# Kernel optimization log

Measured on AMD Instinct MI355X. Metric: run time of the kernel, lower is better.

Reference implementation:

```python
import jax, jax.numpy as jnp
import numpy as np


def setup_inputs() -> dict:
    key = jax.random.key(0)
    kq, kk, kv = jax.random.split(key, 3)
    n, d = 8192, 128
    Q = jax.random.normal(kq, (n, d), dtype=jnp.float32)
    K = jax.random.normal(kk, (n, d), dtype=jnp.float32)
    V = jax.random.normal(kv, (n, d), dtype=jnp.float32)
    return {"Q": Q, "K": K, "V": V}


def reference(Q, K, V):
    # The blockwise online-softmax loops in the torch module compute exactly
    # softmax(Q @ K^T) @ V  -- note: NO 1/sqrt(d) scaling in the original.
    S = jnp.einsum('qd,kd->qk', Q, K)          # [n, n] scores
    P = jax.nn.softmax(S, axis=-1)             # numerically stable softmax
    O = jnp.einsum('qk,kd->qd', P, V)          # [n, d]
    return O
```

## Files before the change

### kernel.cpp

```cpp
#include <hip/hip_runtime.h>
#include <hip/hip_bf16.h>

#define N 8192
#define D 128
#define NSPLIT 8
#define KVSPLIT (N / NSPLIT)
#define KVBLK 64
#define NT (KVSPLIT / KVBLK)

typedef __attribute__((ext_vector_type(8))) _Float16 half8;
typedef __attribute__((ext_vector_type(2))) __fp16 fp16x2;
typedef __attribute__((ext_vector_type(16))) float f32x16;

union H8 { fp16x2 h2[4]; half8 h8; };

__global__ void cvt_f16_4(const float4* __restrict__ src, _Float16* __restrict__ dst, int n4) {
    int i = blockIdx.x * 256 + threadIdx.x;
    if (i < n4) {
        float4 v = src[i];
        _Float16 o0 = (_Float16)v.x, o1 = (_Float16)v.y, o2 = (_Float16)v.z, o3 = (_Float16)v.w;
        ushort4 o;
        o.x = __builtin_bit_cast(ushort, o0);
        o.y = __builtin_bit_cast(ushort, o1);
        o.z = __builtin_bit_cast(ushort, o2);
        o.w = __builtin_bit_cast(ushort, o3);
        *reinterpret_cast<ushort4*>(dst + i * 4) = o;
    }
}

__global__ void transpose_v(const float* __restrict__ V, _Float16* __restrict__ Vtp) {
    __shared__ _Float16 tile[64][65];
    const int k0 = blockIdx.x * 64;
    const int d0 = blockIdx.y * 64;
    const int tid = threadIdx.x;
#pragma unroll
    for (int p = 0; p < 16; ++p) {
        int flat = p * 256 + tid;
        int r = flat >> 6, cc = flat & 63;
        tile[r][cc] = (_Float16)(V[(size_t)(k0 + r) * D + d0 + cc]);
    }
    __syncthreads();
#pragma unroll
    for (int p = 0; p < 16; ++p) {
        int flat = p * 256 + tid;
        int dd = flat >> 6, kl = flat & 63;
        int kk = kl & 31;
        int s32 = 16 * (kk >> 4) + 8 * ((kk >> 2) & 1) + 4 * ((kk >> 3) & 1) + (kk & 3);
        Vtp[(size_t)(d0 + dd) * N + k0 + (kl & 32) + s32] = tile[kl][dd];
    }
}

#define STAGE(kdst_, vdst_, kbase_)                                                   \
    {                                                                                 \
        _Pragma("unroll")                                                             \
        for (int p = 0; p < 4; ++p) {                                                 \
            int c4 = p * 256 + tid;                                                   \
            int row = c4 >> 4, chs = c4 & 15;                                         \
            int cc = (chs & 8) | ((chs & 7) ^ (row & 7));                             \
            __builtin_amdgcn_global_load_lds(                                         \
                (const __attribute__((address_space(1))) void*)(Kh + (size_t)((kbase_) + row) * D + cc * 8), \
                (__attribute__((address_space(3))) void*)((kdst_) + c4 * 8), 16, 0, 0);              \
        }                                                                             \
        _Pragma("unroll")                                                             \
        for (int p = 0; p < 4; ++p) {                                                 \
            int c4 = p * 256 + tid;                                                   \
            int dd = c4 >> 3, chs = c4 & 7;                                           \
            int cc = chs ^ (dd & 7);                                                  \
            __builtin_amdgcn_global_load_lds(                                         \
                (const __attribute__((address_space(1))) void*)(Vtp + (size_t)dd * N + (kbase_) + cc * 8),   \
                (__attribute__((address_space(3))) void*)((vdst_) + c4 * 8), 16, 0, 0);              \
        }                                                                             \
    }

#define PVSTEP(Pv, ktc)                                                               \
    _Pragma("unroll")                                                                 \
    for (int ks = 0; ks < 2; ++ks) {                                                  \
        H8 u;                                                                         \
        u.h2[0] = __builtin_amdgcn_cvt_pkrtz(Pv[ks * 8 + 0], Pv[ks * 8 + 1]);         \
        u.h2[1] = __builtin_amdgcn_cvt_pkrtz(Pv[ks * 8 + 2], Pv[ks * 8 + 3]);         \
        u.h2[2] = __builtin_amdgcn_cvt_pkrtz(Pv[ks * 8 + 4], Pv[ks * 8 + 5]);         \
        u.h2[3] = __builtin_amdgcn_cvt_pkrtz(Pv[ks * 8 + 6], Pv[ks * 8 + 7]);         \
        int ch = (ktc) * 4 + ks * 2 + h;                                              \
        _Pragma("unroll")                                                             \
        for (int dt = 0; dt < 4; ++dt) {                                              \
            int dd = dt * 32 + c;                                                     \
            int pos = ch ^ (dd & 7);                                                  \
            half8 vf = *reinterpret_cast<const half8*>(vb + dd * 64 + pos * 8);       \
            oacc[dt] = __builtin_amdgcn_mfma_f32_32x32x16_f16(vf, u.h8, oacc[dt], 0, 0, 0); \
        }                                                                             \
    }

__launch_bounds__(256, 2)
__global__ void fa_kernel(const _Float16* __restrict__ Qh, const _Float16* __restrict__ Kh,
                          const _Float16* __restrict__ Vtp, _Float16* __restrict__ Oph,
                          float* __restrict__ Mpart, float* __restrict__ Lpart) {
    __shared__ __align__(16) _Float16 smem[32768];

    const int tid  = threadIdx.x;
    const int w    = tid >> 6;
    const int lane = tid & 63;
    const int h    = lane >> 5;
    const int c    = lane & 31;
    const int bid  = blockIdx.x;
    const int split = bid & 7;
    const int bx   = bid >> 3;
    const int q0w  = bx * 128 + w * 32;
    const int kv0  = split * KVSPLIT;

    half8 qa[8];
    {
        const _Float16* qrow = Qh + (size_t)(q0w + c) * D + h * 8;
#pragma unroll
        for (int st = 0; st < 8; ++st)
            qa[st] = *reinterpret_cast<const half8*>(qrow + st * 16);
    }

    f32x16 oacc[4];
#pragma unroll
    for (int dt = 0; dt < 4; ++dt)
#pragma unroll
        for (int r = 0; r < 16; ++r) oacc[dt][r] = 0.f;
    float mrun = -1e30f, lrun = 0.f;

    STAGE(smem, smem + 16384, kv0);
    __syncthreads();

    for (int t = 0; t < NT; ++t) {
        const int cur = t & 1;
        if (t + 1 < NT)
            STAGE(smem + (cur ^ 1) * 8192, smem + 16384 + (cur ^ 1) * 8192, kv0 + (t + 1) * KVBLK);

        const _Float16* kb = smem + cur * 8192;
        const _Float16* vb = smem + 16384 + cur * 8192;

        f32x16 sb0, sb1;
#pragma unroll
        for (int r = 0; r < 16; ++r) { sb0[r] = 0.f; sb1[r] = 0.f; }
#pragma unroll
        for (int st = 0; st < 8; ++st) {
            int ch = st * 2 + h;
            int pos = (ch & 8) | ((ch & 7) ^ (c & 7));
            half8 kf0 = *reinterpret_cast<const half8*>(kb + c * 128 + pos * 8);
            half8 kf1 = *reinterpret_cast<const half8*>(kb + (32 + c) * 128 + pos * 8);
            sb0 = __builtin_amdgcn_mfma_f32_32x32x16_f16(kf0, qa[st], sb0, 0, 0, 0);
            sb1 = __builtin_amdgcn_mfma_f32_32x32x16_f16(kf1, qa[st], sb1, 0, 0, 0);
        }

        float pmax = sb0[0];
#pragma unroll
        for (int r = 1; r < 16; ++r) pmax = fmaxf(pmax, sb0[r]);
#pragma unroll
        for (int r = 0; r < 16; ++r) pmax = fmaxf(pmax, sb1[r]);
        pmax = fmaxf(pmax, __shfl_xor(pmax, 32));

        if (!__all(pmax <= mrun + 8.0f)) {
            float nm = fmaxf(mrun, pmax);
            float scl = __expf(mrun - nm);
            lrun *= scl;
#pragma unroll
            for (int dt = 0; dt < 4; ++dt)
#pragma unroll
                for (int r = 0; r < 16; ++r) oacc[dt][r] *= scl;
            mrun = nm;
        }
        float tsum = 0.f;
#pragma unroll
        for (int r = 0; r < 16; ++r) { sb0[r] = __expf(sb0[r] - mrun); tsum += sb0[r]; }
#pragma unroll
        for (int r = 0; r < 16; ++r) { sb1[r] = __expf(sb1[r] - mrun); tsum += sb1[r]; }
        lrun += tsum + __shfl_xor(tsum, 32);

        PVSTEP(sb0, 0)
        PVSTEP(sb1, 1)

        __syncthreads();
    }

    __syncthreads();
    float inv = 1.0f / lrun;
    float* epi = reinterpret_cast<float*>(smem) + w * 1088;
    const size_t sbase = (size_t)split * N;
#pragma unroll
    for (int dt = 0; dt < 4; ++dt) {
#pragma unroll
        for (int r = 0; r < 16; ++r) {
            int dloc = (r & 3) + 8 * (r >> 2) + 4 * h;
            epi[c * 33 + dloc] = oacc[dt][r] * inv;
        }
#pragma unroll
        for (int it = 0; it < 16; ++it) {
            int j = it * 64 + lane;
            int rr = j >> 5, cc2 = j & 31;
            Oph[(sbase + q0w + rr) * D + dt * 32 + cc2] = (_Float16)epi[rr * 33 + cc2];
        }
    }
    if (h == 0) {
        Mpart[sbase + q0w + c] = mrun;
        Lpart[sbase + q0w + c] = lrun;
    }
}

__global__ void fa_merge(const _Float16* __restrict__ Oph, const float* __restrict__ Mpart,
                         const float* __restrict__ Lpart, float* __restrict__ O) {
    int idx = blockIdx.x * 256 + threadIdx.x;
    int q = idx >> 7;
    int d = idx & 127;
    float m[NSPLIT];
    float M = -1e30f;
#pragma unroll
    for (int s = 0; s < NSPLIT; ++s) {
        m[s] = Mpart[s * N + q];
        M = fmaxf(M, m[s]);
    }
    float acc = 0.f, wsum = 0.f;
#pragma unroll
    for (int s = 0; s < NSPLIT; ++s) {
        float wgt = __expf(m[s] - M) * Lpart[s * N + q];
        acc += wgt * (float)Oph[((size_t)s * N + q) * D + d];
        wsum += wgt;
    }
    O[idx] = acc / wsum;
}

extern "C" void kernel_launch(void* const* d_in, const int* in_sizes, int n_in,
                              void* d_out, int out_size, void* d_ws, size_t ws_size,
                              hipStream_t stream) {
    const float* Q = (const float*)d_in[0];
    const float* K = (const float*)d_in[1];
    const float* V = (const float*)d_in[2];
    float* O = (float*)d_out;

    _Float16* Qh = (_Float16*)d_ws;
    _Float16* Kh = Qh + (size_t)N * D;
    _Float16* Vtp = Kh + (size_t)N * D;
    _Float16* Oph = Vtp + (size_t)N * D;
    float* Mpart = (float*)(Oph + (size_t)NSPLIT * N * D);
    float* Lpart = Mpart + (size_t)NSPLIT * N;

    const int n4 = N * D / 4;
    hipLaunchKernelGGL(cvt_f16_4, dim3(n4 / 256), dim3(256), 0, stream,
                       (const float4*)Q, Qh, n4);
    hipLaunchKernelGGL(cvt_f16_4, dim3(n4 / 256), dim3(256), 0, stream,
                       (const float4*)K, Kh, n4);
    hipLaunchKernelGGL(transpose_v, dim3(N / 64, D / 64), dim3(256), 0, stream, V, Vtp);
    hipLaunchKernelGGL(fa_kernel, dim3(64 * NSPLIT), dim3(256), 0, stream,
                       Qh, Kh, Vtp, Oph, Mpart, Lpart);
    hipLaunchKernelGGL(fa_merge, dim3(N * D / 256), dim3(256), 0, stream,
                       Oph, Mpart, Lpart, O);
}
```

Before: 64.32 us.

## Software-pipeline PV matmul with triple-buffered V and fuse prep kernels

Merges the Q/K conversion and V transpose kernels into a single prep launch. The attention loop now defers each tile's PV MFMA into the next iteration, using a triple-buffered V tile in shared memory (LDS grows to 80KB), so it overlaps with the QK^T MFMAs. Wave priority is raised around the MFMA section. It also switches exponentials to raw v_exp_f32 with a folded log2e FMA and uses tree reductions for the max and sum. The extra LDS could limit occupancy to two blocks per CU, and the deferred P fragments add register pressure.

```diff
diff --git a/kernel.cpp b/kernel.cpp
--- a/kernel.cpp
+++ b/kernel.cpp
@@ -7,6 +7,7 @@
 #define KVSPLIT (N / NSPLIT)
 #define KVBLK 64
 #define NT (KVSPLIT / KVBLK)
+#define L2E 1.442695041f
 
 typedef __attribute__((ext_vector_type(8))) _Float16 half8;
 typedef __attribute__((ext_vector_type(2))) __fp16 fp16x2;
@@ -14,43 +15,54 @@
 
 union H8 { fp16x2 h2[4]; half8 h8; };
 
-__global__ void cvt_f16_4(const float4* __restrict__ src, _Float16* __restrict__ dst, int n4) {
-    int i = blockIdx.x * 256 + threadIdx.x;
-    if (i < n4) {
-        float4 v = src[i];
-        _Float16 o0 = (_Float16)v.x, o1 = (_Float16)v.y, o2 = (_Float16)v.z, o3 = (_Float16)v.w;
-        ushort4 o;
-        o.x = __builtin_bit_cast(ushort, o0);
-        o.y = __builtin_bit_cast(ushort, o1);
-        o.z = __builtin_bit_cast(ushort, o2);
-        o.w = __builtin_bit_cast(ushort, o3);
-        *reinterpret_cast<ushort4*>(dst + i * 4) = o;
-    }
-}
-
-__global__ void transpose_v(const float* __restrict__ V, _Float16* __restrict__ Vtp) {
+__device__ __forceinline__ float fexp2(float x) {
+    float r; asm("v_exp_f32 %0, %1" : "=v"(r) : "v"(x)); return r;
+}
+
+__global__ void prep_kernel(const float* __restrict__ Q, const float* __restrict__ K,
+                            const float* __restrict__ V, _Float16* __restrict__ Qh,
+                            _Float16* __restrict__ Kh, _Float16* __restrict__ Vtp) {
     __shared__ _Float16 tile[64][65];
-    const int k0 = blockIdx.x * 64;
-    const int d0 = blockIdx.y * 64;
+    const int bid = blockIdx.x;
     const int tid = threadIdx.x;
-#pragma unroll
-    for (int p = 0; p < 16; ++p) {
-        int flat = p * 256 + tid;
-        int r = flat >> 6, cc = flat & 63;
-        tile[r][cc] = (_Float16)(V[(size_t)(k0 + r) * D + d0 + cc]);
-    }
-    __syncthreads();
-#pragma unroll
-    for (int p = 0; p < 16; ++p) {
-        int flat = p * 256 + tid;
-        int dd = flat >> 6, kl = flat & 63;
-        int kk = kl & 31;
-        int s32 = 16 * (kk >> 4) + 8 * ((kk >> 2) & 1) + 4 * ((kk >> 3) & 1) + (kk & 3);
-        Vtp[(size_t)(d0 + dd) * N + k0 + (kl & 32) + s32] = tile[kl][dd];
-    }
-}
-
-#define STAGE(kdst_, vdst_, kbase_)                                                   \
+    if (bid < 1024) {
+        const float4* src = (const float4*)(bid < 512 ? Q : K);
+        _Float16* dst = (bid < 512) ? Qh : Kh;
+        const int b = bid & 511;
+#pragma unroll
+        for (int p = 0; p < 2; ++p) {
+            int i = b * 512 + p * 256 + tid;
+            float4 v = src[i];
+            ushort4 o;
+            o.x = __builtin_bit_cast(ushort, (_Float16)v.x);
+            o.y = __builtin_bit_cast(ushort, (_Float16)v.y);
+            o.z = __builtin_bit_cast(ushort, (_Float16)v.z);
+            o.w = __builtin_bit_cast(ushort, (_Float16)v.w);
+            *reinterpret_cast<ushort4*>(dst + (size_t)i * 4) = o;
+        }
+    } else {
+        const int vbid = bid - 1024;
+        const int k0 = (vbid & 127) * 64;
+        const int d0 = (vbid >> 7) * 64;
+#pragma unroll
+        for (int p = 0; p < 16; ++p) {
+            int flat = p * 256 + tid;
+            int r = flat >> 6, cc = flat & 63;
+            tile[r][cc] = (_Float16)(V[(size_t)(k0 + r) * D + d0 + cc]);
+        }
+        __syncthreads();
+#pragma unroll
+        for (int p = 0; p < 16; ++p) {
+            int flat = p * 256 + tid;
+            int dd = flat >> 6, kl = flat & 63;
+            int kk = kl & 31;
+            int s32 = 16 * (kk >> 4) + 8 * ((kk >> 2) & 1) + 4 * ((kk >> 3) & 1) + (kk & 3);
+            Vtp[(size_t)(d0 + dd) * N + k0 + (kl & 32) + s32] = tile[kl][dd];
+        }
+    }
+}
+
+#define STAGE_K(kdst_, kbase_)                                                        \
     {                                                                                 \
         _Pragma("unroll")                                                             \
         for (int p = 0; p < 4; ++p) {                                                 \
@@ -61,6 +73,9 @@
                 (const __attribute__((address_space(1))) void*)(Kh + (size_t)((kbase_) + row) * D + cc * 8), \
                 (__attribute__((address_space(3))) void*)((kdst_) + c4 * 8), 16, 0, 0);              \
         }                                                                             \
+    }
+#define STAGE_V(vdst_, kbase_)                                                        \
+    {                                                                                 \
         _Pragma("unroll")                                                             \
         for (int p = 0; p < 4; ++p) {                                                 \
             int c4 = p * 256 + tid;                                                   \
@@ -72,21 +87,16 @@
         }                                                                             \
     }
 
-#define PVSTEP(Pv, ktc)                                                               \
+#define PV_ALL(vb_)                                                                   \
     _Pragma("unroll")                                                                 \
-    for (int ks = 0; ks < 2; ++ks) {                                                  \
-        H8 u;                                                                         \
-        u.h2[0] = __builtin_amdgcn_cvt_pkrtz(Pv[ks * 8 + 0], Pv[ks * 8 + 1]);         \
-        u.h2[1] = __builtin_amdgcn_cvt_pkrtz(Pv[ks * 8 + 2], Pv[ks * 8 + 3]);         \
-        u.h2[2] = __builtin_amdgcn_cvt_pkrtz(Pv[ks * 8 + 4], Pv[ks * 8 + 5]);         \
-        u.h2[3] = __builtin_amdgcn_cvt_pkrtz(Pv[ks * 8 + 6], Pv[ks * 8 + 7]);         \
-        int ch = (ktc) * 4 + ks * 2 + h;                                              \
+    for (int j = 0; j < 4; ++j) {                                                     \
+        int ch = j * 2 + h;                                                           \
         _Pragma("unroll")                                                             \
         for (int dt = 0; dt < 4; ++dt) {                                              \
             int dd = dt * 32 + c;                                                     \
             int pos = ch ^ (dd & 7);                                                  \
-            half8 vf = *reinterpret_cast<const half8*>(vb + dd * 64 + pos * 8);       \
-            oacc[dt] = __builtin_amdgcn_mfma_f32_32x32x16_f16(vf, u.h8, oacc[dt], 0, 0, 0); \
+            half8 vf = *reinterpret_cast<const half8*>((vb_) + dd * 64 + pos * 8);    \
+            oacc[dt] = __builtin_amdgcn_mfma_f32_32x32x16_f16(vf, pk[j].h8, oacc[dt], 0, 0, 0); \
         }                                                                             \
     }
 
@@ -94,7 +104,7 @@
 __global__ void fa_kernel(const _Float16* __restrict__ Qh, const _Float16* __restrict__ Kh,
                           const _Float16* __restrict__ Vtp, _Float16* __restrict__ Oph,
                           float* __restrict__ Mpart, float* __restrict__ Lpart) {
-    __shared__ __align__(16) _Float16 smem[32768];
+    __shared__ __align__(16) _Float16 smem[40960];
 
     const int tid  = threadIdx.x;
     const int w    = tid >> 6;
@@ -107,6 +117,11 @@
     const int q0w  = bx * 128 + w * 32;
     const int kv0  = split * KVSPLIT;
 
+    _Float16* const kb0 = smem;
+    _Float16* const vbA = smem + 16384;
+    _Float16* const vbB = smem + 24576;
+    _Float16* const vbC = smem + 32768;
+
     half8 qa[8];
     {
         const _Float16* qrow = Qh + (size_t)(q0w + c) * D + h * 8;
@@ -121,41 +136,49 @@
 #pragma unroll
         for (int r = 0; r < 16; ++r) oacc[dt][r] = 0.f;
     float mrun = -1e30f, lrun = 0.f;
-
-    STAGE(smem, smem + 16384, kv0);
+    H8 pk[4];
+
+    STAGE_K(kb0, kv0);
+    STAGE_V(vbA, kv0);
     __syncthreads();
 
+    _Float16 *vprev = vbC, *vcur = vbA, *vstage = vbB;
+
     for (int t = 0; t < NT; ++t) {
-        const int cur = t & 1;
-        if (t + 1 < NT)
-            STAGE(smem + (cur ^ 1) * 8192, smem + 16384 + (cur ^ 1) * 8192, kv0 + (t + 1) * KVBLK);
-
-        const _Float16* kb = smem + cur * 8192;
-        const _Float16* vb = smem + 16384 + cur * 8192;
+        _Float16* kcur = kb0 + (t & 1) * 8192;
+        if (t + 1 < NT) {
+            STAGE_K(kb0 + ((t + 1) & 1) * 8192, kv0 + (t + 1) * KVBLK);
+            STAGE_V(vstage, kv0 + (t + 1) * KVBLK);
+        }
 
         f32x16 sb0, sb1;
 #pragma unroll
         for (int r = 0; r < 16; ++r) { sb0[r] = 0.f; sb1[r] = 0.f; }
+        __builtin_amdgcn_s_setprio(1);
 #pragma unroll
         for (int st = 0; st < 8; ++st) {
             int ch = st * 2 + h;
             int pos = (ch & 8) | ((ch & 7) ^ (c & 7));
-            half8 kf0 = *reinterpret_cast<const half8*>(kb + c * 128 + pos * 8);
-            half8 kf1 = *reinterpret_cast<const half8*>(kb + (32 + c) * 128 + pos * 8);
+            half8 kf0 = *reinterpret_cast<const half8*>(kcur + c * 128 + pos * 8);
+            half8 kf1 = *reinterpret_cast<const half8*>(kcur + (32 + c) * 128 + pos * 8);
             sb0 = __builtin_amdgcn_mfma_f32_32x32x16_f16(kf0, qa[st], sb0, 0, 0, 0);
             sb1 = __builtin_amdgcn_mfma_f32_32x32x16_f16(kf1, qa[st], sb1, 0, 0, 0);
         }
-
-        float pmax = sb0[0];
-#pragma unroll
-        for (int r = 1; r < 16; ++r) pmax = fmaxf(pmax, sb0[r]);
-#pragma unroll
-        for (int r = 0; r < 16; ++r) pmax = fmaxf(pmax, sb1[r]);
-        pmax = fmaxf(pmax, __shfl_xor(pmax, 32));
+        if (t > 0) { PV_ALL(vprev) }
+        __builtin_amdgcn_s_setprio(0);
+
+        float mx[16];
+#pragma unroll
+        for (int r = 0; r < 16; ++r) mx[r] = fmaxf(sb0[r], sb1[r]);
+#pragma unroll
+        for (int s = 8; s > 0; s >>= 1)
+#pragma unroll
+            for (int r = 0; r < s; ++r) mx[r] = fmaxf(mx[r], mx[r + s]);
+        float pmax = fmaxf(mx[0], __shfl_xor(mx[0], 32));
 
         if (!__all(pmax <= mrun + 8.0f)) {
             float nm = fmaxf(mrun, pmax);
-            float scl = __expf(mrun - nm);
+            float scl = fexp2((mrun - nm) * L2E);
             lrun *= scl;
 #pragma unroll
             for (int dt = 0; dt < 4; ++dt)
@@ -163,18 +186,35 @@
                 for (int r = 0; r < 16; ++r) oacc[dt][r] *= scl;
             mrun = nm;
         }
-        float tsum = 0.f;
-#pragma unroll
-        for (int r = 0; r < 16; ++r) { sb0[r] = __expf(sb0[r] - mrun); tsum += sb0[r]; }
-#pragma unroll
-        for (int r = 0; r < 16; ++r) { sb1[r] = __expf(sb1[r] - mrun); tsum += sb1[r]; }
-        lrun += tsum + __shfl_xor(tsum, 32);
-
-        PVSTEP(sb0, 0)
-        PVSTEP(sb1, 1)
+        const float nml = -mrun * L2E;
+#pragma unroll
+        for (int r = 0; r < 16; ++r) sb0[r] = fexp2(__builtin_fmaf(sb0[r], L2E, nml));
+#pragma unroll
+        for (int r = 0; r < 16; ++r) sb1[r] = fexp2(__builtin_fmaf(sb1[r], L2E, nml));
+        float ts[16];
+#pragma unroll
+        for (int r = 0; r < 16; ++r) ts[r] = sb0[r] + sb1[r];
+#pragma unroll
+        for (int s = 8; s > 0; s >>= 1)
+#pragma unroll
+            for (int r = 0; r < s; ++r) ts[r] += ts[r + s];
+        lrun += ts[0] + __shfl_xor(ts[0], 32);
+
+#pragma unroll
+        for (int i = 0; i < 4; ++i) {
+            pk[0].h2[i] = __builtin_amdgcn_cvt_pkrtz(sb0[2 * i], sb0[2 * i + 1]);
+            pk[1].h2[i] = __builtin_amdgcn_cvt_pkrtz(sb0[8 + 2 * i], sb0[8 + 2 * i + 1]);
+            pk[2].h2[i] = __builtin_amdgcn_cvt_pkrtz(sb1[2 * i], sb1[2 * i + 1]);
+            pk[3].h2[i] = __builtin_amdgcn_cvt_pkrtz(sb1[8 + 2 * i], sb1[8 + 2 * i + 1]);
+        }
 
         __syncthreads();
-    }
+        _Float16* tmp = vprev; vprev = vcur; vcur = vstage; vstage = tmp;
+    }
+
+    __builtin_amdgcn_s_setprio(1);
+    PV_ALL(vprev)
+    __builtin_amdgcn_s_setprio(0);
 
     __syncthreads();
     float inv = 1.0f / lrun;
@@ -215,7 +255,7 @@
     float acc = 0.f, wsum = 0.f;
 #pragma unroll
     for (int s = 0; s < NSPLIT; ++s) {
-        float wgt = __expf(m[s] - M) * Lpart[s * N + q];
+        float wgt = fexp2((m[s] - M) * L2E) * Lpart[s * N + q];
         acc += wgt * (float)Oph[((size_t)s * N + q) * D + d];
         wsum += wgt;
     }
@@ -237,13 +277,9 @@
     float* Mpart = (float*)(Oph + (size_t)NSPLIT * N * D);
     float* Lpart = Mpart + (size_t)NSPLIT * N;
 
-    const int n4 = N * D / 4;
-    hipLaunchKernelGGL(cvt_f16_4, dim3(n4 / 256), dim3(256), 0, stream,
-                       (const float4*)Q, Qh, n4);
-    hipLaunchKernelGGL(cvt_f16_4, dim3(n4 / 256), dim3(256), 0, stream,
-                       (const float4*)K, Kh, n4);
-    hipLaunchKernelGGL(transpose_v, dim3(N / 64, D / 64), dim3(256), 0, stream, V, Vtp);
-    hipLaunchKernelGGL(fa_kernel, dim3(64 * NSPLIT), dim3(256), 0, stream,
+    hipLaunchKernelGGL(prep_kernel, dim3(1280), dim3(256), 0, stream,
+                       Q, K, V, Qh, Kh, Vtp);
+    hipLaunchKernelGGL(fa_kernel, dim3((N / 128) * NSPLIT), dim3(256), 0, stream,
                        Qh, Kh, Vtp, Oph, Mpart, Lpart);
     hipLaunchKernelGGL(fa_merge, dim3(N * D / 256), dim3(256), 0, stream,
                        Oph, Mpart, Lpart, O);
```

After: 59.09 us. -8.1%, faster.
